# Performance work log

Hardware: AMD Instinct MI355X
Metric: run time of the kernel (lower is better)

Reference implementation:

```python
import math
import jax, jax.numpy as jnp
import numpy as np

CAPACITY_FACTOR = 1.25  # _DEFAULT_EP_CAPACITY_FACTOR
STD = 0.02


def setup_inputs() -> dict:
    key = jax.random.key(0)
    k_x, k_r, k_ug, k_d = jax.random.split(key, 4)
    B, S, D, E, I = 8, 4096, 1024, 16, 2816
    x = jax.random.normal(k_x, (B, S, D), dtype=jnp.float32)
    router = STD * jax.random.truncated_normal(k_r, -3, 3, (D, E)).astype(jnp.float32)
    w_up_gate = STD * jax.random.truncated_normal(k_ug, -3, 3, (E, D, 2 * I)).astype(jnp.float32)
    w_down = STD * jax.random.truncated_normal(k_d, -3, 3, (E, I, D)).astype(jnp.float32)
    return {"x": x, "router": router, "w_up_gate": w_up_gate, "w_down": w_down,
            "num_experts_per_token": 2}


def _routing_stats(selected_experts, router_probs, router_logits, num_experts, k):
    probs = router_probs.astype(jnp.float32)
    logits = router_logits.astype(jnp.float32)
    expert_counts = jnp.sum(jax.nn.one_hot(selected_experts, num_experts, dtype=jnp.float32), axis=(0, 1))
    total = jnp.maximum(jnp.sum(expert_counts), 1.0)
    frac = expert_counts / total
    entropy = -jnp.sum(frac * jnp.log(frac + 1e-06))
    token_fraction = frac * k
    p = jnp.mean(probs, axis=0)
    lb_loss = num_experts * jnp.sum(token_fraction * p)
    z = jax.scipy.special.logsumexp(logits, axis=-1)
    z_loss = jnp.mean(z ** 2)
    return expert_counts, entropy, lb_loss, z_loss


def _moe_forward(x, router, w_up_gate, w_down, k):
    B, S, D = x.shape
    E = router.shape[1]
    T = B * S
    x_flat = x.reshape(T, D)

    router_logits = jnp.einsum('td,de->te', x_flat, router)          # [T,E]
    router_probs = jax.nn.softmax(router_logits, axis=-1)
    topk_logits, selected = jax.lax.top_k(router_logits, k)          # [T,K]
    combine = jax.nn.softmax(topk_logits, axis=-1).astype(x.dtype)   # [T,K]

    stats = _routing_stats(selected, router_probs, router_logits, E, k)

    # ---- capacity-based dispatch ----
    C = int(math.ceil(T * k / E * CAPACITY_FACTOR))                  # static
    TK = T * k
    flat_sel = selected.reshape(TK).astype(jnp.int32)                # token-major priority
    oh = jax.nn.one_hot(flat_sel, E, dtype=jnp.int32)                # [TK,E]
    pos = jnp.take_along_axis(jnp.cumsum(oh, axis=0), flat_sel[:, None], axis=1)[:, 0] - 1
    keep = pos < C                                                   # [TK]
    pos_safe = jnp.where(keep, pos, 0)
    token_idx = jnp.arange(TK, dtype=jnp.int32) // k

    vals = jnp.where(keep[:, None], x_flat[token_idx], 0.0)          # [TK,D]
    expert_in = jnp.zeros((E, C, D), dtype=x.dtype).at[flat_sel, pos_safe].add(vals)

    # ---- grouped SwiGLU MLP ----
    h = jnp.einsum('ecd,edf->ecf', expert_in, w_up_gate)             # [E,C,2I]
    I = w_down.shape[1]
    gate, up = h[..., :I], h[..., I:]
    act = jax.nn.silu(gate) * up                                     # [E,C,I]
    expert_out = jnp.einsum('eci,eid->ecd', act, w_down)             # [E,C,D]

    # ---- combine ----
    gathered = expert_out[flat_sel, pos_safe]                        # [TK,D]
    w = (combine.reshape(TK) * keep.astype(x.dtype))[:, None]
    routed = (gathered * w).reshape(T, k, D).sum(axis=1)             # [T,D]
    return routed.reshape(B, S, D), stats


def reference(x, router, w_up_gate, w_down, num_experts_per_token):
    routed, (counts, entropy, lb_loss, z_loss) = _moe_forward(
        x, router, w_up_gate, w_down, num_experts_per_token)
    return routed, counts, entropy, lb_loss, z_loss
```

## Files before the change

### kernel.cpp

```cpp
#include <hip/hip_runtime.h>
#include <math.h>

#define T_TOK 32768
#define TKA   65536
#define DIM   1024
#define NE    16
#define IDIM  2816
#define CAP   5120

typedef short short8 __attribute__((ext_vector_type(8)));
typedef float floatx4 __attribute__((ext_vector_type(4)));

__device__ __forceinline__ unsigned short f2bf(float f) {
  unsigned int u = __float_as_uint(f);
  u = u + 0x7FFFu + ((u >> 16) & 1u);
  return (unsigned short)(u >> 16);
}
__device__ __forceinline__ float bf2f(unsigned short h) {
  return __uint_as_float(((unsigned int)h) << 16);
}

__device__ __forceinline__ void gld_lds16(const void* g, void* l) {
  __builtin_amdgcn_global_load_lds(
      (const __attribute__((address_space(1))) unsigned int*)(unsigned long long)g,
      (__attribute__((address_space(3))) unsigned int*)(unsigned int)(unsigned long long)l,
      16, 0, 0);
}


__global__ void cvtx_kernel(const float* __restrict__ in, unsigned short* __restrict__ out) {
  size_t i = ((size_t)blockIdx.x * 256 + threadIdx.x) * 8;
  float4 a = *(const float4*)(in + i);
  float4 b = *(const float4*)(in + i + 4);
  short8 v;
  v[0] = (short)f2bf(a.x); v[1] = (short)f2bf(a.y); v[2] = (short)f2bf(a.z); v[3] = (short)f2bf(a.w);
  v[4] = (short)f2bf(b.x); v[5] = (short)f2bf(b.y); v[6] = (short)f2bf(b.z); v[7] = (short)f2bf(b.w);
  *(short8*)(out + i) = v;
}

__global__ void transpose_cvt(const float* __restrict__ in, unsigned short* __restrict__ out,
                              int R, int Cin) {
  int e = blockIdx.z;
  size_t base = (size_t)e * R * Cin;
  int ct = blockIdx.x;
  int rt = blockIdx.y;
  __shared__ unsigned short Ts[64][72];
  int tx = threadIdx.x & 63, ty = threadIdx.x >> 6;
#pragma unroll
  for (int j = 0; j < 16; j++) {
    int r = rt * 64 + ty + j * 4;
    int c = ct * 64 + tx;
    Ts[tx][ty + j * 4] = f2bf(in[base + (size_t)r * Cin + c]);
  }
  __syncthreads();
#pragma unroll
  for (int j = 0; j < 16; j++) {
    int cl = ty + j * 4;
    out[base + (size_t)(ct * 64 + cl) * R + rt * 64 + tx] = Ts[cl][tx];
  }
}


__global__ void router_kernel(const float* __restrict__ x, const float* __restrict__ router,
                              float* __restrict__ logits) {
  int tid = blockIdx.x * 256 + threadIdx.x;
  int tk = tid >> 4, e = tid & 15;
  const float* xr = x + (size_t)tk * DIM;
  float acc = 0.f;
#pragma unroll 8
  for (int d = 0; d < DIM; d++) acc = fmaf(xr[d], router[d * NE + e], acc);
  logits[tid] = acc;
}

__global__ void topk_kernel(const float* __restrict__ logits, int* __restrict__ sel,
                            float* __restrict__ wcomb, float* __restrict__ prob_sums,
                            int* __restrict__ counts_raw, float* __restrict__ z2sum) {
  __shared__ float ps[16];
  __shared__ int   cs[16];
  __shared__ float zs;
  int tid = threadIdx.x;
  if (tid < 16) { ps[tid] = 0.f; cs[tid] = 0; }
  if (tid == 0) zs = 0.f;
  __syncthreads();
  int t = blockIdx.x * 256 + tid;
  float l[16];
#pragma unroll
  for (int e = 0; e < 16; e++) l[e] = logits[(size_t)t * 16 + e];
  float m1 = l[0]; int e1 = 0;
#pragma unroll
  for (int e = 1; e < 16; e++) if (l[e] > m1) { m1 = l[e]; e1 = e; }
  float m2 = -3.4e38f; int e2 = 0;
#pragma unroll
  for (int e = 0; e < 16; e++) if (e != e1 && l[e] > m2) { m2 = l[e]; e2 = e; }
  float b  = __expf(m2 - m1);
  float w1 = 1.f / (1.f + b);
  sel[t * 2] = e1; sel[t * 2 + 1] = e2;
  wcomb[t * 2] = w1; wcomb[t * 2 + 1] = 1.f - w1;
  float s = 0.f;
  float pexp[16];
#pragma unroll
  for (int e = 0; e < 16; e++) { pexp[e] = __expf(l[e] - m1); s += pexp[e]; }
  float inv = 1.f / s;
#pragma unroll
  for (int e = 0; e < 16; e++) atomicAdd(&ps[e], pexp[e] * inv);
  atomicAdd(&cs[e1], 1); atomicAdd(&cs[e2], 1);
  float z = m1 + __logf(s);
  atomicAdd(&zs, z * z);
  __syncthreads();
  if (tid < 16) { atomicAdd(&prob_sums[tid], ps[tid]); atomicAdd(&counts_raw[tid], cs[tid]); }
  if (tid == 0) atomicAdd(z2sum, zs);
}

__global__ void hist_kernel(const int* __restrict__ sel, int* __restrict__ bhist) {
  __shared__ int h[16];
  int tid = threadIdx.x;
  if (tid < 16) h[tid] = 0;
  __syncthreads();
  atomicAdd(&h[sel[blockIdx.x * 256 + tid]], 1);
  __syncthreads();
  if (tid < 16) bhist[blockIdx.x * 16 + tid] = h[tid];
}

__global__ void scan_kernel(const int* __restrict__ bhist, int* __restrict__ bbase,
                            int* __restrict__ capc) {
  __shared__ int h[256 * 16];
  int t = threadIdx.x;
  for (int i = t; i < 256 * 16 / 4; i += 256)
    ((int4*)h)[i] = ((const int4*)bhist)[i];
  __syncthreads();
  if (t < 16) {
    int run = 0;
    for (int b = 0; b < 256; b++) { bbase[b * 16 + t] = run; run += h[b * 16 + t]; }
    capc[t] = run < CAP ? run : CAP;
  }
}

__global__ void rank_kernel(const int* __restrict__ sel, const int* __restrict__ bbase,
                            int* __restrict__ pos_tk, int* __restrict__ scat) {
  __shared__ int se[256];
  int i = threadIdx.x;
  int a = blockIdx.x * 256 + i;
  int e = sel[a];
  se[i] = e;
  __syncthreads();
  int r = 0;
  for (int j = 0; j < i; j++) r += (se[j] == e) ? 1 : 0;
  int pos = bbase[blockIdx.x * 16 + e] + r;
  if (pos < CAP) { pos_tk[a] = pos; scat[e * CAP + pos] = a >> 1; }
  else           { pos_tk[a] = -1; }
}


__global__ __launch_bounds__(256) void gemm1_kernel(
    const unsigned short* __restrict__ xb, const unsigned short* __restrict__ wtg,
    const int* __restrict__ scat, const int* __restrict__ capc,
    const unsigned short* __restrict__ zrow, unsigned short* __restrict__ act) {
  int e = blockIdx.z, ct = blockIdx.x, it = blockIdx.y;
  if (ct * 128 >= capc[e]) return;
  __shared__ __align__(16) unsigned short As0[128 * 64], As1[128 * 64];
  __shared__ __align__(16) unsigned short Bg0[64 * 64],  Bg1[64 * 64];
  __shared__ __align__(16) unsigned short Bu0[64 * 64],  Bu1[64 * 64];
  const int t = threadIdx.x, w = t >> 6, l = t & 63;
  const int lr8   = l >> 3;
  const int koffs = ((l & 7) ^ lr8) * 8;

  const unsigned short* aptr[4];
#pragma unroll
  for (int j = 0; j < 4; j++) {
    int c0 = ct * 128 + w * 32 + j * 8 + lr8;
    int tok = scat[e * CAP + c0];
    aptr[j] = (tok >= 0 ? xb + (size_t)tok * DIM : zrow) + koffs;
  }
  const unsigned short* bgp[2];
  const unsigned short* bup[2];
#pragma unroll
  for (int j = 0; j < 2; j++) {
    int n0 = it * 64 + w * 16 + j * 8 + lr8;
    bgp[j] = wtg + ((size_t)e * (2 * IDIM) + n0) * DIM + koffs;
    bup[j] = bgp[j] + (size_t)IDIM * DIM;
  }

  floatx4 accg[8], accu[8];
#pragma unroll
  for (int i = 0; i < 8; i++) {
    accg[i] = (floatx4){0.f, 0.f, 0.f, 0.f};
    accu[i] = (floatx4){0.f, 0.f, 0.f, 0.f};
  }
  const int wm = w >> 1, wn = w & 1;
  const int rl = l & 15, lq = l >> 4, sx = l & 7;

  auto stage = [&](int k0, unsigned short* As, unsigned short* Bg, unsigned short* Bu) {
#pragma unroll
    for (int j = 0; j < 4; j++)
      gld_lds16(aptr[j] + k0, (char*)As + w * 4096 + j * 1024);
#pragma unroll
    for (int j = 0; j < 2; j++) {
      gld_lds16(bgp[j] + k0, (char*)Bg + w * 2048 + j * 1024);
      gld_lds16(bup[j] + k0, (char*)Bu + w * 2048 + j * 1024);
    }
  };
  auto compute = [&](const unsigned short* As, const unsigned short* Bg,
                     const unsigned short* Bu) {
#pragma unroll
    for (int ks = 0; ks < 2; ks++) {
      const int slot = ((ks * 4 + lq) ^ sx) * 8;
      short8 af[4], bgf[2], buf2[2];
#pragma unroll
      for (int mi = 0; mi < 4; mi++)
        af[mi] = *(const short8*)(As + (wm * 64 + mi * 16 + rl) * 64 + slot);
#pragma unroll
      for (int ni = 0; ni < 2; ni++) {
        bgf[ni]  = *(const short8*)(Bg + (wn * 32 + ni * 16 + rl) * 64 + slot);
        buf2[ni] = *(const short8*)(Bu + (wn * 32 + ni * 16 + rl) * 64 + slot);
      }
#pragma unroll
      for (int mi = 0; mi < 4; mi++)
#pragma unroll
        for (int ni = 0; ni < 2; ni++) {
          accg[mi * 2 + ni] = __builtin_amdgcn_mfma_f32_16x16x32_bf16(af[mi], bgf[ni],  accg[mi * 2 + ni], 0, 0, 0);
          accu[mi * 2 + ni] = __builtin_amdgcn_mfma_f32_16x16x32_bf16(af[mi], buf2[ni], accu[mi * 2 + ni], 0, 0, 0);
        }
    }
  };

  stage(0, As0, Bg0, Bu0);
  __syncthreads();
  for (int k0 = 0; k0 < DIM; k0 += 128) {
    stage(k0 + 64, As1, Bg1, Bu1);
    compute(As0, Bg0, Bu0);
    __syncthreads();
    if (k0 + 128 < DIM) stage(k0 + 128, As0, Bg0, Bu0);
    compute(As1, Bg1, Bu1);
    __syncthreads();
  }

  size_t abase = ((size_t)e * CAP + (size_t)ct * 128) * IDIM + (size_t)it * 64;
#pragma unroll
  for (int mi = 0; mi < 4; mi++)
#pragma unroll
    for (int reg = 0; reg < 4; reg++) {
      int m = wm * 64 + mi * 16 + lq * 4 + reg;
#pragma unroll
      for (int ni = 0; ni < 2; ni++) {
        int n = wn * 32 + ni * 16 + (l & 15);
        float g = accg[mi * 2 + ni][reg];
        float u = accu[mi * 2 + ni][reg];
        float a = g / (1.f + __expf(-g)) * u;
        act[abase + (size_t)m * IDIM + n] = f2bf(a);
      }
    }
}


__global__ __launch_bounds__(256) void gemm2_kernel(
    const unsigned short* __restrict__ act, const unsigned short* __restrict__ wtd,
    const int* __restrict__ capc, unsigned short* __restrict__ eout) {
  int e = blockIdx.z, ct = blockIdx.x, it = blockIdx.y;
  if (ct * 128 >= capc[e]) return;
  __shared__ __align__(16) unsigned short As0[128 * 64], As1[128 * 64];
  __shared__ __align__(16) unsigned short Bs0[64 * 64],  Bs1[64 * 64];
  const int t = threadIdx.x, w = t >> 6, l = t & 63;
  const int lr8   = l >> 3;
  const int koffs = ((l & 7) ^ lr8) * 8;

  const unsigned short* aptr[4];
#pragma unroll
  for (int j = 0; j < 4; j++)
    aptr[j] = act + ((size_t)e * CAP + ct * 128 + w * 32 + j * 8 + lr8) * IDIM + koffs;
  const unsigned short* bptr[2];
#pragma unroll
  for (int j = 0; j < 2; j++)
    bptr[j] = wtd + ((size_t)e * DIM + it * 64 + w * 16 + j * 8 + lr8) * IDIM + koffs;

  floatx4 acc[8];
#pragma unroll
  for (int i = 0; i < 8; i++) acc[i] = (floatx4){0.f, 0.f, 0.f, 0.f};
  const int wm = w >> 1, wn = w & 1;
  const int rl = l & 15, lq = l >> 4, sx = l & 7;

  auto stage = [&](int k0, unsigned short* As, unsigned short* Bs) {
#pragma unroll
    for (int j = 0; j < 4; j++)
      gld_lds16(aptr[j] + k0, (char*)As + w * 4096 + j * 1024);
#pragma unroll
    for (int j = 0; j < 2; j++)
      gld_lds16(bptr[j] + k0, (char*)Bs + w * 2048 + j * 1024);
  };
  auto compute = [&](const unsigned short* As, const unsigned short* Bs) {
#pragma unroll
    for (int ks = 0; ks < 2; ks++) {
      const int slot = ((ks * 4 + lq) ^ sx) * 8;
      short8 af[4], bf2[2];
#pragma unroll
      for (int mi = 0; mi < 4; mi++)
        af[mi] = *(const short8*)(As + (wm * 64 + mi * 16 + rl) * 64 + slot);
#pragma unroll
      for (int ni = 0; ni < 2; ni++)
        bf2[ni] = *(const short8*)(Bs + (wn * 32 + ni * 16 + rl) * 64 + slot);
#pragma unroll
      for (int mi = 0; mi < 4; mi++)
#pragma unroll
        for (int ni = 0; ni < 2; ni++)
          acc[mi * 2 + ni] = __builtin_amdgcn_mfma_f32_16x16x32_bf16(af[mi], bf2[ni], acc[mi * 2 + ni], 0, 0, 0);
    }
  };

  stage(0, As0, Bs0);
  __syncthreads();
  for (int k0 = 0; k0 < IDIM; k0 += 128) {
    stage(k0 + 64, As1, Bs1);
    compute(As0, Bs0);
    __syncthreads();
    if (k0 + 128 < IDIM) stage(k0 + 128, As0, Bs0);
    compute(As1, Bs1);
    __syncthreads();
  }

  size_t obase = ((size_t)e * CAP + (size_t)ct * 128) * DIM + (size_t)it * 64;
#pragma unroll
  for (int mi = 0; mi < 4; mi++)
#pragma unroll
    for (int reg = 0; reg < 4; reg++) {
      int m = wm * 64 + mi * 16 + lq * 4 + reg;
#pragma unroll
      for (int ni = 0; ni < 2; ni++) {
        int n = wn * 32 + ni * 16 + (l & 15);
        eout[obase + (size_t)m * DIM + n] = f2bf(acc[mi * 2 + ni][reg]);
      }
    }
}


__global__ void combine_kernel(const unsigned short* __restrict__ eout,
                               const int* __restrict__ sel, const int* __restrict__ pos_tk,
                               const float* __restrict__ wcomb, float* __restrict__ routed) {
  int tok = blockIdx.x;
  int d = threadIdx.x * 4;
  float a0 = 0.f, a1 = 0.f, a2 = 0.f, a3 = 0.f;
#pragma unroll
  for (int s = 0; s < 2; s++) {
    int a = tok * 2 + s;
    int p = pos_tk[a];
    if (p >= 0) {
      int e = sel[a];
      float wgt = wcomb[a];
      const unsigned short* row = eout + ((size_t)e * CAP + p) * DIM + d;
      ushort4 r = *(const ushort4*)row;
      a0 += wgt * bf2f(r.x); a1 += wgt * bf2f(r.y);
      a2 += wgt * bf2f(r.z); a3 += wgt * bf2f(r.w);
    }
  }
  float4 o = {a0, a1, a2, a3};
  *(float4*)(routed + (size_t)tok * DIM + d) = o;
}

__global__ void finalize_kernel(const int* __restrict__ counts_raw, const float* __restrict__ psums,
                                const float* __restrict__ z2sum, float* __restrict__ tail) {
  if (threadIdx.x != 0 || blockIdx.x != 0) return;
  float ent = 0.f, lb = 0.f;
  for (int e = 0; e < 16; e++) {
    float c = (float)counts_raw[e];
    tail[e] = c;
    float frac = c / 65536.f;
    ent -= frac * logf(frac + 1e-6f);
    lb += frac * 2.f * (psums[e] / 32768.f);
  }
  tail[16] = ent;
  tail[17] = 16.f * lb;
  tail[18] = z2sum[0] / 32768.f;
}


extern "C" void kernel_launch(void* const* d_in, const int* in_sizes, int n_in,
                              void* d_out, int out_size, void* d_ws, size_t ws_size,
                              hipStream_t stream) {
  (void)in_sizes; (void)n_in; (void)out_size; (void)ws_size;
  const float* x         = (const float*)d_in[0];
  const float* router    = (const float*)d_in[1];
  const float* w_up_gate = (const float*)d_in[2];
  const float* w_down    = (const float*)d_in[3];
  float* out = (float*)d_out;

  char* p = (char*)d_ws;
  size_t off = 0;
  auto alc = [&](size_t n) { void* r = p + off; off += (n + 255) & ~(size_t)255; return r; };

  unsigned short* xb   = (unsigned short*)alc((size_t)T_TOK * DIM * 2);
  unsigned short* wtg  = (unsigned short*)alc((size_t)NE * 2 * IDIM * DIM * 2);
  unsigned short* wtd  = (unsigned short*)alc((size_t)NE * DIM * IDIM * 2);
  unsigned short* act  = (unsigned short*)alc((size_t)NE * CAP * IDIM * 2);
  unsigned short* eout = (unsigned short*)alc((size_t)NE * CAP * DIM * 2);
  float* logits = (float*)alc((size_t)T_TOK * NE * 4);
  int*   sel    = (int*)alc((size_t)TKA * 4);
  float* wcomb  = (float*)alc((size_t)TKA * 4);
  int*   pos_tk = (int*)alc((size_t)TKA * 4);
  int*   scat   = (int*)alc((size_t)NE * CAP * 4);
  int*   bhist  = (int*)alc(256 * 16 * 4);
  int*   bbase  = (int*)alc(256 * 16 * 4);
  int*   capc   = (int*)alc(64);
  int*   counts_raw = (int*)alc(64);
  float* psums  = (float*)alc(64);
  float* z2     = (float*)alc(64);
  unsigned short* zrow = (unsigned short*)alc(DIM * 2);

  hipMemsetAsync(counts_raw, 0, 64, stream);
  hipMemsetAsync(psums, 0, 64, stream);
  hipMemsetAsync(z2, 0, 64, stream);
  hipMemsetAsync(scat, 0xFF, (size_t)NE * CAP * 4, stream);
  hipMemsetAsync(zrow, 0, DIM * 2, stream);

  cvtx_kernel<<<T_TOK * DIM / (256 * 8), 256, 0, stream>>>(x, xb);
  transpose_cvt<<<dim3(2 * IDIM / 64, DIM / 64, NE), 256, 0, stream>>>(w_up_gate, wtg, DIM, 2 * IDIM);
  transpose_cvt<<<dim3(DIM / 64, IDIM / 64, NE), 256, 0, stream>>>(w_down, wtd, IDIM, DIM);

  router_kernel<<<T_TOK * NE / 256, 256, 0, stream>>>(x, router, logits);
  topk_kernel<<<T_TOK / 256, 256, 0, stream>>>(logits, sel, wcomb, psums, counts_raw, z2);
  hist_kernel<<<TKA / 256, 256, 0, stream>>>(sel, bhist);
  scan_kernel<<<1, 256, 0, stream>>>(bhist, bbase, capc);
  rank_kernel<<<TKA / 256, 256, 0, stream>>>(sel, bbase, pos_tk, scat);

  gemm1_kernel<<<dim3(CAP / 128, IDIM / 64, NE), 256, 0, stream>>>(xb, wtg, scat, capc, zrow, act);
  gemm2_kernel<<<dim3(CAP / 128, DIM / 64, NE), 256, 0, stream>>>(act, wtd, capc, eout);

  combine_kernel<<<T_TOK, 256, 0, stream>>>(eout, sel, pos_tk, wcomb, out);
  finalize_kernel<<<1, 64, 0, stream>>>(counts_raw, psums, z2, out + (size_t)T_TOK * DIM);
}
```

Measured before the change: 2.351 ms.

## Use partial vmcnt waits with raw barriers to overlap LDS loads in GEMMs

Replaces __syncthreads in the double-buffered up/gate and down GEMM main loops with s_barrier preceded by partial s_waitcnt vmcnt, so the next stage's global-to-LDS loads can stay in flight while the current buffer is consumed. Sched barriers pin instruction order around the barriers. The point is to avoid the full vmcnt(0) drain that __syncthreads implies. The cost is hand-counted outstanding-load numbers (8 and 6), which must match exactly how many loads each stage issues, otherwise stale data is read.

Result: no change. 2.335 ms (-0.7%).

```diff
diff --git a/kernel.cpp b/kernel.cpp
--- a/kernel.cpp
+++ b/kernel.cpp
@@ -25,6 +25,35 @@
       (const __attribute__((address_space(1))) unsigned int*)(unsigned long long)g,
       (__attribute__((address_space(3))) unsigned int*)(unsigned int)(unsigned long long)l,
       16, 0, 0);
+}
+
+__device__ __forceinline__ void sbar() {
+  __builtin_amdgcn_sched_barrier(0);
+  asm volatile("" ::: "memory");
+  __builtin_amdgcn_s_barrier();
+  asm volatile("" ::: "memory");
+  __builtin_amdgcn_sched_barrier(0);
+}
+__device__ __forceinline__ void sbar_vm8() {
+  __builtin_amdgcn_sched_barrier(0);
+  asm volatile("s_waitcnt vmcnt(8)" ::: "memory");
+  __builtin_amdgcn_s_barrier();
+  asm volatile("" ::: "memory");
+  __builtin_amdgcn_sched_barrier(0);
+}
+__device__ __forceinline__ void sbar_vm6() {
+  __builtin_amdgcn_sched_barrier(0);
+  asm volatile("s_waitcnt vmcnt(6)" ::: "memory");
+  __builtin_amdgcn_s_barrier();
+  asm volatile("" ::: "memory");
+  __builtin_amdgcn_sched_barrier(0);
+}
+__device__ __forceinline__ void sbar_vm0() {
+  __builtin_amdgcn_sched_barrier(0);
+  asm volatile("s_waitcnt vmcnt(0)" ::: "memory");
+  __builtin_amdgcn_s_barrier();
+  asm volatile("" ::: "memory");
+  __builtin_amdgcn_sched_barrier(0);
 }
 
 
@@ -223,16 +252,24 @@
     }
   };
 
+  const int NT = DIM / 64;
   stage(0, As0, Bg0, Bu0);
-  __syncthreads();
-  for (int k0 = 0; k0 < DIM; k0 += 128) {
-    stage(k0 + 64, As1, Bg1, Bu1);
+  int tt = 0;
+  for (; tt + 2 < NT; tt += 2) {
+    stage((tt + 1) * 64, As1, Bg1, Bu1);
+    sbar_vm8();
     compute(As0, Bg0, Bu0);
-    __syncthreads();
-    if (k0 + 128 < DIM) stage(k0 + 128, As0, Bg0, Bu0);
+    sbar();
+    stage((tt + 2) * 64, As0, Bg0, Bu0);
+    sbar_vm8();
     compute(As1, Bg1, Bu1);
-    __syncthreads();
-  }
+    sbar();
+  }
+  stage((NT - 1) * 64, As1, Bg1, Bu1);
+  sbar_vm8();
+  compute(As0, Bg0, Bu0);
+  sbar_vm0();
+  compute(As1, Bg1, Bu1);
 
   size_t abase = ((size_t)e * CAP + (size_t)ct * 128) * IDIM + (size_t)it * 64;
 #pragma unroll
@@ -305,16 +342,24 @@
     }
   };
 
+  const int NT = IDIM / 64;
   stage(0, As0, Bs0);
-  __syncthreads();
-  for (int k0 = 0; k0 < IDIM; k0 += 128) {
-    stage(k0 + 64, As1, Bs1);
+  int tt = 0;
+  for (; tt + 2 < NT; tt += 2) {
+    stage((tt + 1) * 64, As1, Bs1);
+    sbar_vm6();
     compute(As0, Bs0);
-    __syncthreads();
-    if (k0 + 128 < IDIM) stage(k0 + 128, As0, Bs0);
+    sbar();
+    stage((tt + 2) * 64, As0, Bs0);
+    sbar_vm6();
     compute(As1, Bs1);
-    __syncthreads();
-  }
+    sbar();
+  }
+  stage((NT - 1) * 64, As1, Bs1);
+  sbar_vm6();
+  compute(As0, Bs0);
+  sbar_vm0();
+  compute(As1, Bs1);
 
   size_t obase = ((size_t)e * CAP + (size_t)ct * 128) * DIM + (size_t)it * 64;
 #pragma unroll
```
